# Kernel optimization log

Hardware: AMD Instinct MI355X
Metric: run time of the kernel (lower is better)

The kernel has to match this reference:

```python
import jax, jax.numpy as jnp
import numpy as np

TAU_SQUARED = 2.0
EPS = 1e-12
B, K = 4096, 128
E, D = 100000, 128


def setup_inputs() -> dict:
    key = jax.random.key(0)
    k1, k2, k3, k4 = jax.random.split(key, 4)
    sq_dists = jax.random.uniform(k1, (B, K), dtype=jnp.float32)
    labels = jax.random.randint(k2, (B, K), 0, E, dtype=jnp.int64)
    log_exemplar_event_counts = jax.random.normal(k3, (E, D), dtype=jnp.float32)
    log_exemplar_censor_counts = jax.random.normal(k4, (E, D), dtype=jnp.float32)
    log_baseline_event_counts = jnp.full((D,), -27.6310211159, dtype=jnp.float32)
    log_baseline_censor_counts = jnp.full((D,), -27.6310211159, dtype=jnp.float32)
    return {
        "sq_dists": sq_dists,
        "log_exemplar_event_counts": log_exemplar_event_counts,
        "log_exemplar_censor_counts": log_exemplar_censor_counts,
        "log_baseline_event_counts": log_baseline_event_counts,
        "log_baseline_censor_counts": log_baseline_censor_counts,
        "labels": labels,
    }


def reference(sq_dists, log_exemplar_event_counts, log_exemplar_censor_counts,
              log_baseline_event_counts, log_baseline_censor_counts, labels):
    # Kernel weights w[b,k] = exp(-d^2) * 1[d^2 <= tau^2]; the original scatters
    # these into a dense [B, E] matrix, but the matmul against [E, D] tables is
    # exactly a k-NN gather + weighted sum (neighbor cols are unique per row).
    w = jnp.exp(-sq_dists) * (sq_dists <= TAU_SQUARED).astype(sq_dists.dtype)  # [B, K]

    exemplar_event_counts = jnp.exp(log_exemplar_event_counts)    # [E, D]
    exemplar_censor_counts = jnp.exp(log_exemplar_censor_counts)  # [E, D]
    # flip -> cumsum -> flip == reversed cumulative sum along durations
    exemplar_at_risk_counts = jnp.cumsum(
        (exemplar_event_counts + exemplar_censor_counts)[:, ::-1], axis=1)[:, ::-1]

    baseline_event_counts = jnp.exp(log_baseline_event_counts)    # [D]
    baseline_censor_counts = jnp.exp(log_baseline_censor_counts)  # [D]
    baseline_at_risk_counts = jnp.cumsum(
        (baseline_event_counts + baseline_censor_counts)[::-1])[::-1]

    ev_g = exemplar_event_counts[labels]       # [B, K, D] gather
    ar_g = exemplar_at_risk_counts[labels]     # [B, K, D] gather
    numer = jnp.einsum('bk,bkd->bd', w, ev_g) + baseline_event_counts[None, :]
    denom = jnp.einsum('bk,bkd->bd', w, ar_g) + baseline_at_risk_counts[None, :] + EPS
    return jnp.clip(numer / denom, EPS, 1.0 - EPS)
```

## Files before the change

kernel.cpp:

```cpp
#include <hip/hip_runtime.h>
#include <hip/hip_fp16.h>
#include <math.h>

#define DD 128
#define TAU2 2.0f
#define EPSV 1e-12f

__global__ void baseline_kernel(const float* __restrict__ log_be,
                                const float* __restrict__ log_bc,
                                float* __restrict__ base_ev,
                                float* __restrict__ base_ar) {
    __shared__ float sm[DD];
    int d = threadIdx.x;
    float be = expf(log_be[d]);
    float bc = expf(log_bc[d]);
    base_ev[d] = be;
    sm[d] = be + bc;
    __syncthreads();
    #pragma unroll
    for (int off = 1; off < DD; off <<= 1) {
        float v = (d + off < DD) ? sm[d + off] : 0.0f;
        __syncthreads();
        sm[d] += v;
        __syncthreads();
    }
    base_ar[d] = sm[d];
}

__global__ __launch_bounds__(256) void prep_kernel(
    const float* __restrict__ log_ev,
    const float* __restrict__ log_cen,
    unsigned short* __restrict__ tab,
    long long c0, long long rows, long long E) {
    int tid = threadIdx.x;
    int lane = tid & 63;
    long long wave = ((long long)blockIdx.x * blockDim.x + tid) >> 6;
    long long nwaves = ((long long)gridDim.x * blockDim.x) >> 6;

    for (long long row = wave; row < rows; row += nwaves) {
        long long e = row + c0;
        size_t idx = ((size_t)e * DD + 2 * lane);
        float2 le = *(const float2*)(log_ev + idx);
        float2 lc = *(const float2*)(log_cen + idx);
        float ea = __expf(le.x), eb = __expf(le.y);
        float a = ea + __expf(lc.x);
        float b = eb + __expf(lc.y);
        float t = a + b;
        #pragma unroll
        for (int off = 1; off < 64; off <<= 1) {
            float v = __shfl_down(t, off, 64);
            t += (lane + off < 64) ? v : 0.0f;
        }
        float ar0 = t;
        float ar1 = t - a;
        __half2 e2 = __floats2half2_rn(ea, eb);
        __half2 a2 = __floats2half2_rn(ar0, ar1);
        uint2 pkt;
        pkt.x = *(unsigned int*)&e2;
        pkt.y = *(unsigned int*)&a2;
        *(uint2*)(tab + (size_t)row * 256 + (size_t)lane * 4) = pkt;
    }
}

__global__ __launch_bounds__(256) void gather_kernel(
    const float* __restrict__ sq_dists,
    const int*   __restrict__ labels,
    const unsigned short* __restrict__ tab,
    const float* __restrict__ base_ev,
    const float* __restrict__ base_ar,
    float* __restrict__ acc_num,
    float* __restrict__ acc_den,
    float* __restrict__ out,
    int K, int c0, int c1, int fused) {
    __shared__ float w_s[256];
    __shared__ int   lab_s[256];
    __shared__ float rn[4][DD];
    __shared__ float rd[4][DD];

    int b = blockIdx.x;
    int tid = threadIdx.x;
    if (tid < K) {
        float sqd = sq_dists[(size_t)b * K + tid];
        w_s[tid]  = (sqd <= TAU2) ? __expf(-sqd) : 0.0f;
        lab_s[tid] = labels[(size_t)b * K + tid];
    }
    __syncthreads();

    int wid = tid >> 6;
    int lane = tid & 63;
    const unsigned short* lbase = tab + (size_t)lane * 4;

    float nx = 0.f, ny = 0.f, dx = 0.f, dy = 0.f;
    if (fused && K == 128) {
        int k0 = wid << 5;
        #pragma unroll 8
        for (int i = 0; i < 32; ++i) {
            int k = k0 + i;
            int l = lab_s[k];
            float wk = w_s[k];
            uint2 pkt = *(const uint2*)(lbase + (size_t)l * 256);
            float2 ef = __half22float2(*(const __half2*)&pkt.x);
            float2 af = __half22float2(*(const __half2*)&pkt.y);
            nx = fmaf(wk, ef.x, nx); ny = fmaf(wk, ef.y, ny);
            dx = fmaf(wk, af.x, dx); dy = fmaf(wk, af.y, dy);
        }
    } else {
        int kpw = (K + 3) >> 2;
        for (int i = 0; i < kpw; ++i) {
            int k = wid * kpw + i;
            if (k >= K) break;
            int l = lab_s[k];
            if (l >= c0 && l < c1) {
                float wk = w_s[k];
                uint2 pkt = *(const uint2*)(lbase + (size_t)(l - c0) * 256);
                float2 ef = __half22float2(*(const __half2*)&pkt.x);
                float2 af = __half22float2(*(const __half2*)&pkt.y);
                nx = fmaf(wk, ef.x, nx); ny = fmaf(wk, ef.y, ny);
                dx = fmaf(wk, af.x, dx); dy = fmaf(wk, af.y, dy);
            }
        }
    }
    int col = lane * 2;
    rn[wid][col] = nx; rn[wid][col + 1] = ny;
    rd[wid][col] = dx; rd[wid][col + 1] = dy;
    __syncthreads();

    if (tid < DD) {
        float n  = rn[0][tid] + rn[1][tid] + rn[2][tid] + rn[3][tid];
        float dn = rd[0][tid] + rd[1][tid] + rd[2][tid] + rd[3][tid];
        size_t o = (size_t)b * DD + tid;
        if (fused) {
            n  += base_ev[tid];
            dn += base_ar[tid] + EPSV;
            float r = n / dn;
            out[o] = fminf(fmaxf(r, EPSV), 1.0f - EPSV);
        } else {
            acc_num[o] += n;
            acc_den[o] += dn;
        }
    }
}

__global__ void finalize_kernel(const float* __restrict__ acc_num,
                                const float* __restrict__ acc_den,
                                const float* __restrict__ base_ev,
                                const float* __restrict__ base_ar,
                                float* __restrict__ out, int total) {
    int i = blockIdx.x * blockDim.x + threadIdx.x;
    if (i >= total) return;
    int d = i & (DD - 1);
    float n  = acc_num[i] + base_ev[d];
    float dn = acc_den[i] + base_ar[d] + EPSV;
    float r = n / dn;
    r = fminf(fmaxf(r, EPSV), 1.0f - EPSV);
    out[i] = r;
}

extern "C" void kernel_launch(void* const* d_in, const int* in_sizes, int n_in,
                              void* d_out, int out_size, void* d_ws, size_t ws_size,
                              hipStream_t stream) {
    const float* sq_dists = (const float*)d_in[0];
    const float* log_ev   = (const float*)d_in[1];
    const float* log_cen  = (const float*)d_in[2];
    const float* log_be   = (const float*)d_in[3];
    const float* log_bc   = (const float*)d_in[4];
    const int*   labels   = (const int*)d_in[5];
    float* out = (float*)d_out;

    const int Dv = in_sizes[3];
    const long long E = (long long)in_sizes[1] / Dv;
    const int B = out_size / Dv;
    const int K = in_sizes[0] / B;

    float* ws = (float*)d_ws;
    float* acc_num = ws;
    float* acc_den = acc_num + (size_t)B * Dv;
    float* base_ev = acc_den + (size_t)B * Dv;
    float* base_ar = base_ev + Dv;
    size_t head_floats = 2 * (size_t)B * Dv + 2 * (size_t)Dv;
    unsigned short* tab = (unsigned short*)(ws + head_floats);

    size_t head_bytes = head_floats * sizeof(float);
    long long cap = 0;
    if (ws_size > head_bytes)
        cap = (long long)((ws_size - head_bytes) / (2 * (size_t)Dv * sizeof(unsigned short)));
    long long chunk = cap > E ? E : cap;
    if (chunk < 1) chunk = 1;

    baseline_kernel<<<1, Dv, 0, stream>>>(log_be, log_bc, base_ev, base_ar);

    if (chunk >= E) {
        prep_kernel<<<2048, 256, 0, stream>>>(log_ev, log_cen, tab, 0, E, E);
        gather_kernel<<<B, 256, 0, stream>>>(sq_dists, labels, tab,
                                             base_ev, base_ar,
                                             acc_num, acc_den, out,
                                             K, 0, (int)E, 1);
    } else {
        hipMemsetAsync(acc_num, 0, 2 * (size_t)B * Dv * sizeof(float), stream);
        for (long long c0 = 0; c0 < E; c0 += chunk) {
            long long c1 = c0 + chunk; if (c1 > E) c1 = E;
            long long rows = c1 - c0;
            prep_kernel<<<2048, 256, 0, stream>>>(log_ev, log_cen, tab, c0, rows, E);
            gather_kernel<<<B, 256, 0, stream>>>(sq_dists, labels, tab,
                                                 base_ev, base_ar,
                                                 acc_num, acc_den, out,
                                                 K, (int)c0, (int)c1, 0);
        }
        finalize_kernel<<<(B * Dv + 255) / 256, 256, 0, stream>>>(
            acc_num, acc_den, base_ev, base_ar, out, B * Dv);
    }
}
```

Measured before the change: 70.35 us.

## Fold baseline into prep kernel and widen row accesses to 16-byte vectors

Removes the separate single-block baseline kernel by computing the baseline exp and reverse cumsum inside block 0 of the prep kernel, saving one launch. Prep and gather now process each table row with half-waves of 32 lanes using float4 loads and 16-byte packed stores and loads, so each wave handles two rows or two neighbors at once. The gather kernel keeps 8 partial accumulators per block instead of 4, with a wider shared-memory reduction. The prep grid is doubled. The aim is fewer, wider memory transactions and more loads in flight, at the cost of more registers and a larger final reduction.

```diff
diff --git a/kernel.cpp b/kernel.cpp
--- a/kernel.cpp
+++ b/kernel.cpp
@@ -6,59 +6,64 @@
 #define TAU2 2.0f
 #define EPSV 1e-12f
 
-__global__ void baseline_kernel(const float* __restrict__ log_be,
-                                const float* __restrict__ log_bc,
-                                float* __restrict__ base_ev,
-                                float* __restrict__ base_ar) {
-    __shared__ float sm[DD];
-    int d = threadIdx.x;
-    float be = expf(log_be[d]);
-    float bc = expf(log_bc[d]);
-    base_ev[d] = be;
-    sm[d] = be + bc;
-    __syncthreads();
-    #pragma unroll
-    for (int off = 1; off < DD; off <<= 1) {
-        float v = (d + off < DD) ? sm[d + off] : 0.0f;
-        __syncthreads();
-        sm[d] += v;
-        __syncthreads();
-    }
-    base_ar[d] = sm[d];
-}
 
 __global__ __launch_bounds__(256) void prep_kernel(
     const float* __restrict__ log_ev,
     const float* __restrict__ log_cen,
+    const float* __restrict__ log_be,
+    const float* __restrict__ log_bc,
     unsigned short* __restrict__ tab,
-    long long c0, long long rows, long long E) {
+    float* __restrict__ base_ev,
+    float* __restrict__ base_ar,
+    long long c0, long long rows, int do_base) {
     int tid = threadIdx.x;
     int lane = tid & 63;
-    long long wave = ((long long)blockIdx.x * blockDim.x + tid) >> 6;
-    long long nwaves = ((long long)gridDim.x * blockDim.x) >> 6;
-
-    for (long long row = wave; row < rows; row += nwaves) {
+    int j = lane & 31;
+    int h = lane >> 5;
+
+    if (do_base && blockIdx.x == 0 && tid < 32) {
+        float4 lb = *(const float4*)(log_be + 4 * j);
+        float4 lc = *(const float4*)(log_bc + 4 * j);
+        float e0 = __expf(lb.x), e1 = __expf(lb.y), e2 = __expf(lb.z), e3 = __expf(lb.w);
+        float s0 = e0 + __expf(lc.x), s1 = e1 + __expf(lc.y);
+        float s2 = e2 + __expf(lc.z), s3 = e3 + __expf(lc.w);
+        float t = s0 + s1 + s2 + s3;
+        #pragma unroll
+        for (int off = 1; off < 32; off <<= 1) {
+            float v = __shfl_down(t, off, 64);
+            t += (j + off < 32) ? v : 0.0f;
+        }
+        *(float4*)(base_ev + 4 * j) = make_float4(e0, e1, e2, e3);
+        *(float4*)(base_ar + 4 * j) = make_float4(t, t - s0, t - s0 - s1, t - s0 - s1 - s2);
+    }
+
+    long long g = (((long long)blockIdx.x * blockDim.x + tid) >> 6) * 2 + h;
+    long long ng = (((long long)gridDim.x * blockDim.x) >> 6) * 2;
+
+    for (long long row = g; row < rows; row += ng) {
         long long e = row + c0;
-        size_t idx = ((size_t)e * DD + 2 * lane);
-        float2 le = *(const float2*)(log_ev + idx);
-        float2 lc = *(const float2*)(log_cen + idx);
-        float ea = __expf(le.x), eb = __expf(le.y);
-        float a = ea + __expf(lc.x);
-        float b = eb + __expf(lc.y);
-        float t = a + b;
+        size_t idx = (size_t)e * DD + 4 * j;
+        float4 le = *(const float4*)(log_ev + idx);
+        float4 lc = *(const float4*)(log_cen + idx);
+        float e0 = __expf(le.x), e1 = __expf(le.y), e2 = __expf(le.z), e3 = __expf(le.w);
+        float s0 = e0 + __expf(lc.x), s1 = e1 + __expf(lc.y);
+        float s2 = e2 + __expf(lc.z), s3 = e3 + __expf(lc.w);
+        float t = s0 + s1 + s2 + s3;
         #pragma unroll
-        for (int off = 1; off < 64; off <<= 1) {
+        for (int off = 1; off < 32; off <<= 1) {
             float v = __shfl_down(t, off, 64);
-            t += (lane + off < 64) ? v : 0.0f;
-        }
-        float ar0 = t;
-        float ar1 = t - a;
-        __half2 e2 = __floats2half2_rn(ea, eb);
-        __half2 a2 = __floats2half2_rn(ar0, ar1);
-        uint2 pkt;
-        pkt.x = *(unsigned int*)&e2;
-        pkt.y = *(unsigned int*)&a2;
-        *(uint2*)(tab + (size_t)row * 256 + (size_t)lane * 4) = pkt;
+            t += (j + off < 32) ? v : 0.0f;
+        }
+        __half2 ep0 = __floats2half2_rn(e0, e1);
+        __half2 ep1 = __floats2half2_rn(e2, e3);
+        __half2 ap0 = __floats2half2_rn(t, t - s0);
+        __half2 ap1 = __floats2half2_rn(t - s0 - s1, t - s0 - s1 - s2);
+        uint4 pkt;
+        pkt.x = *(unsigned int*)&ep0;
+        pkt.y = *(unsigned int*)&ep1;
+        pkt.z = *(unsigned int*)&ap0;
+        pkt.w = *(unsigned int*)&ap1;
+        *(uint4*)(tab + (size_t)row * 256 + (size_t)j * 8) = pkt;
     }
 }
 
@@ -72,10 +77,10 @@
     float* __restrict__ acc_den,
     float* __restrict__ out,
     int K, int c0, int c1, int fused) {
-    __shared__ float w_s[256];
-    __shared__ int   lab_s[256];
-    __shared__ float rn[4][DD];
-    __shared__ float rd[4][DD];
+    __shared__ float w_s[128];
+    __shared__ int   lab_s[128];
+    __shared__ float rn[8][DD];
+    __shared__ float rd[8][DD];
 
     int b = blockIdx.x;
     int tid = threadIdx.x;
@@ -88,46 +93,60 @@
 
     int wid = tid >> 6;
     int lane = tid & 63;
-    const unsigned short* lbase = tab + (size_t)lane * 4;
-
-    float nx = 0.f, ny = 0.f, dx = 0.f, dy = 0.f;
+    int j = lane & 31;
+    int h = lane >> 5;
+    const unsigned short* jbase = tab + (size_t)j * 8;
+
+    float n0 = 0.f, n1 = 0.f, n2 = 0.f, n3 = 0.f;
+    float d0 = 0.f, d1 = 0.f, d2 = 0.f, d3 = 0.f;
+
     if (fused && K == 128) {
         int k0 = wid << 5;
-        #pragma unroll 8
-        for (int i = 0; i < 32; ++i) {
-            int k = k0 + i;
+        #pragma unroll
+        for (int i = 0; i < 16; ++i) {
+            int k = k0 + 2 * i + h;
             int l = lab_s[k];
             float wk = w_s[k];
-            uint2 pkt = *(const uint2*)(lbase + (size_t)l * 256);
-            float2 ef = __half22float2(*(const __half2*)&pkt.x);
-            float2 af = __half22float2(*(const __half2*)&pkt.y);
-            nx = fmaf(wk, ef.x, nx); ny = fmaf(wk, ef.y, ny);
-            dx = fmaf(wk, af.x, dx); dy = fmaf(wk, af.y, dy);
+            uint4 pkt = *(const uint4*)(jbase + (size_t)l * 256);
+            float2 e01 = __half22float2(*(const __half2*)&pkt.x);
+            float2 e23 = __half22float2(*(const __half2*)&pkt.y);
+            float2 a01 = __half22float2(*(const __half2*)&pkt.z);
+            float2 a23 = __half22float2(*(const __half2*)&pkt.w);
+            n0 = fmaf(wk, e01.x, n0); n1 = fmaf(wk, e01.y, n1);
+            n2 = fmaf(wk, e23.x, n2); n3 = fmaf(wk, e23.y, n3);
+            d0 = fmaf(wk, a01.x, d0); d1 = fmaf(wk, a01.y, d1);
+            d2 = fmaf(wk, a23.x, d2); d3 = fmaf(wk, a23.y, d3);
         }
     } else {
         int kpw = (K + 3) >> 2;
-        for (int i = 0; i < kpw; ++i) {
-            int k = wid * kpw + i;
+        for (int kk = h; kk < kpw; kk += 2) {
+            int k = wid * kpw + kk;
             if (k >= K) break;
             int l = lab_s[k];
             if (l >= c0 && l < c1) {
                 float wk = w_s[k];
-                uint2 pkt = *(const uint2*)(lbase + (size_t)(l - c0) * 256);
-                float2 ef = __half22float2(*(const __half2*)&pkt.x);
-                float2 af = __half22float2(*(const __half2*)&pkt.y);
-                nx = fmaf(wk, ef.x, nx); ny = fmaf(wk, ef.y, ny);
-                dx = fmaf(wk, af.x, dx); dy = fmaf(wk, af.y, dy);
+                uint4 pkt = *(const uint4*)(jbase + (size_t)(l - c0) * 256);
+                float2 e01 = __half22float2(*(const __half2*)&pkt.x);
+                float2 e23 = __half22float2(*(const __half2*)&pkt.y);
+                float2 a01 = __half22float2(*(const __half2*)&pkt.z);
+                float2 a23 = __half22float2(*(const __half2*)&pkt.w);
+                n0 = fmaf(wk, e01.x, n0); n1 = fmaf(wk, e01.y, n1);
+                n2 = fmaf(wk, e23.x, n2); n3 = fmaf(wk, e23.y, n3);
+                d0 = fmaf(wk, a01.x, d0); d1 = fmaf(wk, a01.y, d1);
+                d2 = fmaf(wk, a23.x, d2); d3 = fmaf(wk, a23.y, d3);
             }
         }
     }
-    int col = lane * 2;
-    rn[wid][col] = nx; rn[wid][col + 1] = ny;
-    rd[wid][col] = dx; rd[wid][col + 1] = dy;
+    int part = wid * 2 + h;
+    *(float4*)&rn[part][4 * j] = make_float4(n0, n1, n2, n3);
+    *(float4*)&rd[part][4 * j] = make_float4(d0, d1, d2, d3);
     __syncthreads();
 
     if (tid < DD) {
-        float n  = rn[0][tid] + rn[1][tid] + rn[2][tid] + rn[3][tid];
-        float dn = rd[0][tid] + rd[1][tid] + rd[2][tid] + rd[3][tid];
+        float n  = rn[0][tid] + rn[1][tid] + rn[2][tid] + rn[3][tid]
+                 + rn[4][tid] + rn[5][tid] + rn[6][tid] + rn[7][tid];
+        float dn = rd[0][tid] + rd[1][tid] + rd[2][tid] + rd[3][tid]
+                 + rd[4][tid] + rd[5][tid] + rd[6][tid] + rd[7][tid];
         size_t o = (size_t)b * DD + tid;
         if (fused) {
             n  += base_ev[tid];
@@ -187,10 +206,9 @@
     long long chunk = cap > E ? E : cap;
     if (chunk < 1) chunk = 1;
 
-    baseline_kernel<<<1, Dv, 0, stream>>>(log_be, log_bc, base_ev, base_ar);
-
     if (chunk >= E) {
-        prep_kernel<<<2048, 256, 0, stream>>>(log_ev, log_cen, tab, 0, E, E);
+        prep_kernel<<<4096, 256, 0, stream>>>(log_ev, log_cen, log_be, log_bc,
+                                              tab, base_ev, base_ar, 0, E, 1);
         gather_kernel<<<B, 256, 0, stream>>>(sq_dists, labels, tab,
                                              base_ev, base_ar,
                                              acc_num, acc_den, out,
@@ -200,7 +218,9 @@
         for (long long c0 = 0; c0 < E; c0 += chunk) {
             long long c1 = c0 + chunk; if (c1 > E) c1 = E;
             long long rows = c1 - c0;
-            prep_kernel<<<2048, 256, 0, stream>>>(log_ev, log_cen, tab, c0, rows, E);
+            prep_kernel<<<4096, 256, 0, stream>>>(log_ev, log_cen, log_be, log_bc,
+                                                  tab, base_ev, base_ar,
+                                                  c0, rows, c0 == 0 ? 1 : 0);
             gather_kernel<<<B, 256, 0, stream>>>(sq_dists, labels, tab,
                                                  base_ev, base_ar,
                                                  acc_num, acc_den, out,
```

After: 65.80 us, median of 2. 1.07x faster.
